# Performance work log

Hardware: AMD Instinct MI355X
Metric: run time of the kernel (lower is better)

The kernel has to match this reference:

```python
import jax, jax.numpy as jnp
import numpy as np

N = 10000      # nodes
E = 160000     # edges (avg degree 16)
D = 128        # channels
H = 4          # heads
C = 128        # per-head dim (PyG: out_channels per head = channels)
HC = H * C
EPS_SOFTMAX = 1e-16
EPS_NORM = 1e-5


def setup_inputs() -> dict:
    key = jax.random.key(0)
    ks = jax.random.split(key, 12)
    s = 1.0 / np.sqrt(D)
    sb = 1.0 / np.sqrt(3 * D)
    return {
        "x": jax.random.normal(ks[0], (N, D), jnp.float32),
        "edge_index": jax.random.randint(ks[1], (2, E), 0, N, dtype=jnp.int64),
        "Wq": jax.random.normal(ks[2], (D, HC), jnp.float32) * s,
        "bq": jnp.zeros((HC,), jnp.float32),
        "Wk": jax.random.normal(ks[3], (D, HC), jnp.float32) * s,
        "bk": jnp.zeros((HC,), jnp.float32),
        "Wv": jax.random.normal(ks[4], (D, HC), jnp.float32) * s,
        "bv": jnp.zeros((HC,), jnp.float32),
        "Wskip": jax.random.normal(ks[5], (D, D), jnp.float32) * s,
        "bskip": jnp.zeros((D,), jnp.float32),
        "Wbeta": jax.random.normal(ks[6], (3 * D,), jnp.float32) * sb,  # lin_beta, bias=False
        "gn_weight": jnp.ones((D,), jnp.float32),
        "gn_bias": jnp.zeros((D,), jnp.float32),
        "gn_mean_scale": jnp.ones((D,), jnp.float32),
    }


def reference(x, edge_index, Wq, bq, Wk, bk, Wv, bv, Wskip, bskip, Wbeta,
              gn_weight, gn_bias, gn_mean_scale):
    n = x.shape[0]
    src, dst = edge_index[0], edge_index[1]  # messages flow src(j) -> dst(i)

    # Projections [N,H,C]
    q = (x @ Wq + bq).reshape(n, H, C)
    k = (x @ Wk + bk).reshape(n, H, C)
    v = (x @ Wv + bv).reshape(n, H, C)

    # Per-edge attention logits [E,H]
    alpha = jnp.einsum('ehc,ehc->eh', q[dst], k[src]) / jnp.sqrt(jnp.float32(C))

    # Segment softmax over incoming edges of each dst node
    amax = jax.ops.segment_max(alpha, dst, num_segments=n)       # [N,H]
    amax = jnp.where(jnp.isfinite(amax), amax, 0.0)
    ex = jnp.exp(alpha - amax[dst])                              # [E,H]
    denom = jax.ops.segment_sum(ex, dst, num_segments=n)         # [N,H]
    attn = ex / (denom[dst] + EPS_SOFTMAX)                       # [E,H]

    # Weighted scatter-aggregate, then mean over heads (concat=False)
    msgs = attn[:, :, None] * v[src]                             # [E,H,C]
    out = jax.ops.segment_sum(msgs, dst, num_segments=n)         # [N,H,C]
    out = out.mean(axis=1)                                       # [N,D]

    # Beta-gated skip (PyG: beta = sigmoid(lin_beta([out, x_r, out - x_r])))
    skip = x @ Wskip + bskip
    beta = jax.nn.sigmoid(jnp.concatenate([out, skip, out - skip], axis=-1) @ Wbeta)
    beta = beta[:, None]
    out = beta * skip + (1.0 - beta) * out

    # GraphNorm (single graph): (x - mean_scale*mean) / sqrt(var + eps) * w + b
    mean = out.mean(axis=0)
    centered = out - gn_mean_scale * mean
    var = (centered * centered).mean(axis=0)
    out = gn_weight * centered / jnp.sqrt(var + EPS_NORM) + gn_bias

    # GELU (exact) + residual (shapes match); dropout is identity in eval
    out = jax.nn.gelu(out, approximate=False)
    return out + x
```

## Files before the change

### kernel.cpp

```cpp
#include <hip/hip_runtime.h>
#include <hip/hip_bf16.h>
#include <math.h>

#define D_DIM 128
#define HC_DIM 512

typedef __attribute__((ext_vector_type(8))) short bf16x8;
typedef __attribute__((ext_vector_type(4))) float f32x4;
typedef __attribute__((ext_vector_type(2))) float f32x2;

static __device__ __forceinline__ unsigned short f2bf(float f) {
  unsigned u = __float_as_uint(f);
  unsigned r = (u + 0x7fffu + ((u >> 16) & 1u)) >> 16;
  return (unsigned short)r;
}
static __device__ __forceinline__ float bflo(unsigned u) {
  return __uint_as_float(u << 16);
}
static __device__ __forceinline__ float bfhi(unsigned u) {
  return __uint_as_float(u & 0xffff0000u);
}

__global__ void prep_kernel(const float* __restrict__ x,
                            const float* __restrict__ Wq, const float* __restrict__ Wk,
                            const float* __restrict__ Wv, const float* __restrict__ Wskip,
                            const float* __restrict__ bq, const float* __restrict__ bk,
                            const float* __restrict__ bv, const float* __restrict__ bskip,
                            unsigned short* __restrict__ xb,
                            unsigned short* __restrict__ wcat,
                            float* __restrict__ bcat,
                            int* __restrict__ zbase, int zwords, int N) {
  int t = blockIdx.x * 256 + threadIdx.x;
  int X4 = N * 32;
  if (t < X4) {
    float4 f = *(const float4*)&x[t * 4];
    ushort4 o;
    o.x = f2bf(f.x); o.y = f2bf(f.y); o.z = f2bf(f.z); o.w = f2bf(f.w);
    *(ushort4*)&xb[t * 4] = o;
  } else if (t < X4 + 1664 * 128) {
    int widx = t - X4;
    if (widx < 3 * 65536) {
      int segi = widx >> 16;
      int r = widx & 65535;
      int kk = r >> 9;
      int m = r & 511;
      const float* W = (segi == 0) ? Wq : (segi == 1) ? Wk : Wv;
      wcat[(size_t)(segi * 512 + m) * 128 + kk] = f2bf(W[kk * 512 + m]);
    } else {
      int r = widx - 3 * 65536;
      int kk = r >> 7;
      int m = r & 127;
      wcat[(size_t)(1536 + m) * 128 + kk] = f2bf(Wskip[kk * 128 + m]);
    }
  } else if (t < X4 + 1664 * 128 + 1664) {
    int b = t - X4 - 1664 * 128;
    bcat[b] = (b < 512) ? bq[b] : (b < 1024) ? bk[b - 512]
            : (b < 1536) ? bv[b - 1024] : bskip[b - 1536];
  } else if (t < X4 + 1664 * 128 + 1664 + zwords) {
    zbase[t - X4 - 1664 * 128 - 1664] = 0;
  }
}

__global__ __launch_bounds__(256) void gemm_mfma_kernel(
    const unsigned short* __restrict__ Xb, const unsigned short* __restrict__ Wt,
    const float* __restrict__ bcat, unsigned short* __restrict__ qb,
    unsigned char* __restrict__ kv8, float* __restrict__ skip, int N) {
  const int tid = threadIdx.x;
  const int wave = tid >> 6, lane = tid & 63;
  const int l16 = lane & 15, quad = lane >> 4;
  const int row0 = (blockIdx.x * 4 + wave) * 64;
  const int col0 = blockIdx.y * 64;

  const unsigned short* xrow[4];
#pragma unroll
  for (int i = 0; i < 4; ++i) {
    int r = row0 + i * 16 + l16;
    if (r >= N) r = N - 1;
    xrow[i] = Xb + (size_t)r * 128;
  }
  const unsigned short* wrow[4];
  float bias[4];
#pragma unroll
  for (int j = 0; j < 4; ++j) {
    int c = col0 + j * 16 + l16;
    wrow[j] = Wt + (size_t)c * 128;
    bias[j] = bcat[c];
  }

  f32x4 acc[4][4] = {};
#pragma unroll
  for (int kk = 0; kk < 4; ++kk) {
    int k0 = kk * 32 + quad * 8;
    bf16x8 a[4], b[4];
#pragma unroll
    for (int i = 0; i < 4; ++i) a[i] = *(const bf16x8*)(xrow[i] + k0);
#pragma unroll
    for (int j = 0; j < 4; ++j) b[j] = *(const bf16x8*)(wrow[j] + k0);
#pragma unroll
    for (int i = 0; i < 4; ++i)
#pragma unroll
      for (int j = 0; j < 4; ++j)
        acc[i][j] = __builtin_amdgcn_mfma_f32_16x16x32_bf16(a[i], b[j], acc[i][j], 0, 0, 0);
  }

  const int kind = (col0 < 512) ? 0 : (col0 < 1536) ? 1 : 2;
#pragma unroll
  for (int i = 0; i < 4; ++i) {
#pragma unroll
    for (int reg = 0; reg < 4; ++reg) {
      int r = row0 + i * 16 + quad * 4 + reg;
      if (r < N) {
#pragma unroll
        for (int j = 0; j < 4; ++j) {
          int cidx = col0 + j * 16 + l16;
          float val = acc[i][j][reg] + bias[j];
          if (kind == 0) {
            qb[(size_t)r * 512 + cidx] = f2bf(val);
          } else if (kind == 1) {
            int pk = __builtin_amdgcn_cvt_pk_fp8_f32(val, val, 0, false);
            kv8[(size_t)r * 1024 + cidx - 512] = (unsigned char)pk;
          } else {
            skip[(size_t)r * 128 + cidx - 1536] = val;
          }
        }
      }
    }
  }
}

__global__ void hist_kernel(const int* __restrict__ dst, int* __restrict__ cnt, int E) {
  int e = blockIdx.x * 256 + threadIdx.x;
  if (e < E) atomicAdd(&cnt[dst[e]], 1);
}

__global__ __launch_bounds__(256) void scan1_kernel(const int* __restrict__ cnt,
                                                    int* __restrict__ off,
                                                    int* __restrict__ bsum, int n) {
  __shared__ int wsum[4];
  int tid = threadIdx.x;
  int i = blockIdx.x * 256 + tid;
  int lane = tid & 63, w = tid >> 6;
  int v = (i < n) ? cnt[i] : 0;
  int x = v;
#pragma unroll
  for (int d = 1; d < 64; d <<= 1) {
    int y = __shfl_up(x, d);
    if (lane >= d) x += y;
  }
  if (lane == 63) wsum[w] = x;
  __syncthreads();
  int wo = 0;
  for (int j = 0; j < w; ++j) wo += wsum[j];
  if (i < n) off[i] = wo + x - v;
  if (tid == 255) bsum[blockIdx.x] = wo + x;
}

__global__ __launch_bounds__(256) void scan23_kernel(int* __restrict__ off,
                                                     const int* __restrict__ bsum,
                                                     int nb, int n) {
  __shared__ int boffs[64];
  int tid = threadIdx.x;
  if (tid < 64) {
    int v = (tid < nb) ? bsum[tid] : 0;
    int x = v;
#pragma unroll
    for (int d = 1; d < 64; d <<= 1) {
      int y = __shfl_up(x, d);
      if (tid >= d) x += y;
    }
    boffs[tid] = x - v;
    if (tid == 63 && blockIdx.x == 0) off[n] = x;
  }
  __syncthreads();
  int i = blockIdx.x * 256 + tid;
  if (i < n) off[i] += boffs[blockIdx.x];
}

__global__ void scatter_kernel(const int* __restrict__ src, const int* __restrict__ dst,
                               const int* __restrict__ off, int* __restrict__ cur,
                               int* __restrict__ bsrc, int E) {
  int e = blockIdx.x * 256 + threadIdx.x;
  if (e < E) {
    int d = dst[e];
    int p = off[d] + atomicAdd(&cur[d], 1);
    bsrc[p] = src[e];
  }
}

__global__ __launch_bounds__(256) void attn_kernel(
    const unsigned short* __restrict__ qb, const unsigned char* __restrict__ kv8,
    const int* __restrict__ off, const int* __restrict__ bsrc,
    unsigned* __restrict__ oh, int N, int nper) {
  int bx = blockIdx.x;
  int head = bx / nper;
  int tid = threadIdx.x;
  int w = tid >> 6, lane = tid & 63;
  int node = (bx - head * nper) * 4 + w;
  if (node >= N) return;
  int g = lane >> 4, j = lane & 15;

  const float qscale = 0.08838834764831845f * 1.4426950408889634f;
  int4 qi = *(const int4*)(qb + (size_t)node * 512 + head * 128 + j * 8);
  float qf0 = bflo(qi.x) * qscale, qf1 = bfhi(qi.x) * qscale;
  float qf2 = bflo(qi.y) * qscale, qf3 = bfhi(qi.y) * qscale;
  float qf4 = bflo(qi.z) * qscale, qf5 = bfhi(qi.z) * qscale;
  float qf6 = bflo(qi.w) * qscale, qf7 = bfhi(qi.w) * qscale;

  const unsigned char* kb = kv8 + head * 128 + j * 8;
  int beg = off[node], end = off[node + 1];
  float lsum = 0.f;
  float o0 = 0.f, o1 = 0.f, o2 = 0.f, o3 = 0.f;
  float o4 = 0.f, o5 = 0.f, o6 = 0.f, o7 = 0.f;

  for (int idx = beg; idx < end; idx += 4) {
    int rem = end - idx;
    int e = bsrc[idx + ((g < rem) ? g : 0)];
    const unsigned char* kp = kb + (size_t)e * 1024;
    uint2 kw = *(const uint2*)kp;
    uint2 vw = *(const uint2*)(kp + 512);
    f32x2 k01 = __builtin_amdgcn_cvt_pk_f32_fp8(kw.x, false);
    f32x2 k23 = __builtin_amdgcn_cvt_pk_f32_fp8(kw.x, true);
    f32x2 k45 = __builtin_amdgcn_cvt_pk_f32_fp8(kw.y, false);
    f32x2 k67 = __builtin_amdgcn_cvt_pk_f32_fp8(kw.y, true);
    float p = qf0 * k01.x + qf1 * k01.y + qf2 * k23.x + qf3 * k23.y +
              qf4 * k45.x + qf5 * k45.y + qf6 * k67.x + qf7 * k67.y;
    p += __shfl_xor(p, 1);
    p += __shfl_xor(p, 2);
    p += __shfl_xor(p, 4);
    p += __shfl_xor(p, 8);
    float a = (g < rem) ? p : -1e30f;
    float wgt = exp2f(a);
    f32x2 v01 = __builtin_amdgcn_cvt_pk_f32_fp8(vw.x, false);
    f32x2 v23 = __builtin_amdgcn_cvt_pk_f32_fp8(vw.x, true);
    f32x2 v45 = __builtin_amdgcn_cvt_pk_f32_fp8(vw.y, false);
    f32x2 v67 = __builtin_amdgcn_cvt_pk_f32_fp8(vw.y, true);
    lsum += wgt;
    o0 += wgt * v01.x; o1 += wgt * v01.y;
    o2 += wgt * v23.x; o3 += wgt * v23.y;
    o4 += wgt * v45.x; o5 += wgt * v45.y;
    o6 += wgt * v67.x; o7 += wgt * v67.y;
  }
  o0 += __shfl_xor(o0, 16); o0 += __shfl_xor(o0, 32);
  o1 += __shfl_xor(o1, 16); o1 += __shfl_xor(o1, 32);
  o2 += __shfl_xor(o2, 16); o2 += __shfl_xor(o2, 32);
  o3 += __shfl_xor(o3, 16); o3 += __shfl_xor(o3, 32);
  o4 += __shfl_xor(o4, 16); o4 += __shfl_xor(o4, 32);
  o5 += __shfl_xor(o5, 16); o5 += __shfl_xor(o5, 32);
  o6 += __shfl_xor(o6, 16); o6 += __shfl_xor(o6, 32);
  o7 += __shfl_xor(o7, 16); o7 += __shfl_xor(o7, 32);
  lsum += __shfl_xor(lsum, 16); lsum += __shfl_xor(lsum, 32);
  float inv = 1.f / (lsum + 1e-16f);
  if (g == 0) {
    unsigned d0 = (unsigned)f2bf(o0 * inv) | ((unsigned)f2bf(o1 * inv) << 16);
    unsigned d1 = (unsigned)f2bf(o2 * inv) | ((unsigned)f2bf(o3 * inv) << 16);
    unsigned d2 = (unsigned)f2bf(o4 * inv) | ((unsigned)f2bf(o5 * inv) << 16);
    unsigned d3 = (unsigned)f2bf(o6 * inv) | ((unsigned)f2bf(o7 * inv) << 16);
    int4 st; st.x = (int)d0; st.y = (int)d1; st.z = (int)d2; st.w = (int)d3;
    *(int4*)(oh + ((size_t)head * N + node) * 64 + j * 4) = st;
  }
}

__global__ __launch_bounds__(256) void combine_kernel(
    const unsigned* __restrict__ oh, const float* __restrict__ skip,
    const float* __restrict__ Wbeta, float* __restrict__ out2,
    float* __restrict__ colsum, float* __restrict__ colsq, int N) {
  int tid = threadIdx.x;
  int lane = tid & 63, w = tid >> 6;
  int wid = blockIdx.x * 4 + w;
  float2 wb0 = *(const float2*)&Wbeta[lane * 2];
  float2 wb1 = *(const float2*)&Wbeta[128 + lane * 2];
  float2 wb2 = *(const float2*)&Wbeta[256 + lane * 2];
  float cs0 = 0.f, cq0 = 0.f, cs1 = 0.f, cq1 = 0.f;
#pragma unroll
  for (int k = 0; k < 4; ++k) {
    int n = wid + k * 2500;
    if (n < N) {
      unsigned h0 = oh[((size_t)0 * N + n) * 64 + lane];
      unsigned h1 = oh[((size_t)1 * N + n) * 64 + lane];
      unsigned h2 = oh[((size_t)2 * N + n) * 64 + lane];
      unsigned h3 = oh[((size_t)3 * N + n) * 64 + lane];
      float a0 = 0.25f * (bflo(h0) + bflo(h1) + bflo(h2) + bflo(h3));
      float a1 = 0.25f * (bfhi(h0) + bfhi(h1) + bfhi(h2) + bfhi(h3));
      float2 s = *(const float2*)&skip[(size_t)n * 128 + lane * 2];
      float p = a0 * wb0.x + s.x * wb1.x + (a0 - s.x) * wb2.x +
                a1 * wb0.y + s.y * wb1.y + (a1 - s.y) * wb2.y;
#pragma unroll
      for (int dmask = 1; dmask < 64; dmask <<= 1) p += __shfl_xor(p, dmask);
      float beta = 1.f / (1.f + __expf(-p));
      float o0 = beta * s.x + (1.f - beta) * a0;
      float o1 = beta * s.y + (1.f - beta) * a1;
      float2 ov; ov.x = o0; ov.y = o1;
      *(float2*)&out2[(size_t)n * 128 + lane * 2] = ov;
      cs0 += o0; cq0 += o0 * o0;
      cs1 += o1; cq1 += o1 * o1;
    }
  }
  __shared__ float red[4][128];
  __shared__ float redq[4][128];
  red[w][lane * 2] = cs0;
  red[w][lane * 2 + 1] = cs1;
  redq[w][lane * 2] = cq0;
  redq[w][lane * 2 + 1] = cq1;
  __syncthreads();
  if (w == 0) {
    int c = lane * 2;
    float s0 = red[0][c] + red[1][c] + red[2][c] + red[3][c];
    float s1 = red[0][c + 1] + red[1][c + 1] + red[2][c + 1] + red[3][c + 1];
    float q0 = redq[0][c] + redq[1][c] + redq[2][c] + redq[3][c];
    float q1 = redq[0][c + 1] + redq[1][c + 1] + redq[2][c + 1] + redq[3][c + 1];
    atomicAdd(&colsum[c], s0);
    atomicAdd(&colsum[c + 1], s1);
    atomicAdd(&colsq[c], q0);
    atomicAdd(&colsq[c + 1], q1);
  }
}

__global__ void final_kernel(const float* __restrict__ out2,
                             const float* __restrict__ colsum,
                             const float* __restrict__ colsq,
                             const float* __restrict__ gnw,
                             const float* __restrict__ gnb,
                             const float* __restrict__ gnms,
                             const float* __restrict__ x,
                             float* __restrict__ y, int total2, float invN) {
  int i = blockIdx.x * 256 + threadIdx.x;
  if (i < total2) {
    int c = (i & 63) * 2;
    float2 cs = *(const float2*)&colsum[c];
    float2 cq = *(const float2*)&colsq[c];
    float2 gw = *(const float2*)&gnw[c];
    float2 gb = *(const float2*)&gnb[c];
    float2 gs = *(const float2*)&gnms[c];
    float mean0 = cs.x * invN, mean1 = cs.y * invN;
    float var0 = cq.x * invN - mean0 * mean0 * gs.x * (2.f - gs.x);
    float var1 = cq.y * invN - mean1 * mean1 * gs.y * (2.f - gs.y);
    float mul0 = gw.x / sqrtf(var0 + 1e-5f);
    float mul1 = gw.y / sqrtf(var1 + 1e-5f);
    float2 o = *(const float2*)&out2[i * 2];
    float2 xx = *(const float2*)&x[i * 2];
    float t0 = (o.x - gs.x * mean0) * mul0 + gb.x;
    float t1 = (o.y - gs.y * mean1) * mul1 + gb.y;
    float g0 = 0.5f * t0 * (1.f + erff(t0 * 0.70710678118654752f));
    float g1 = 0.5f * t1 * (1.f + erff(t1 * 0.70710678118654752f));
    float2 r; r.x = g0 + xx.x; r.y = g1 + xx.y;
    *(float2*)&y[i * 2] = r;
  }
}

extern "C" void kernel_launch(void* const* d_in, const int* in_sizes, int n_in,
                              void* d_out, int out_size, void* d_ws, size_t ws_size,
                              hipStream_t stream) {
  const float* x     = (const float*)d_in[0];
  const int*   ei    = (const int*)d_in[1];
  const float* Wq    = (const float*)d_in[2];
  const float* bq    = (const float*)d_in[3];
  const float* Wk    = (const float*)d_in[4];
  const float* bk    = (const float*)d_in[5];
  const float* Wv    = (const float*)d_in[6];
  const float* bv    = (const float*)d_in[7];
  const float* Wskip = (const float*)d_in[8];
  const float* bskip = (const float*)d_in[9];
  const float* Wbeta = (const float*)d_in[10];
  const float* gnw   = (const float*)d_in[11];
  const float* gnb   = (const float*)d_in[12];
  const float* gnms  = (const float*)d_in[13];

  const int N = in_sizes[0] / D_DIM;
  const int E = in_sizes[1] / 2;
  const int* src = ei;
  const int* dst = ei + E;

  char* p = (char*)d_ws;
  unsigned short* qb  = (unsigned short*)p; p += (size_t)N * 512 * 2;
  unsigned char*  kv8 = (unsigned char*)p;  p += (size_t)N * 1024;
  unsigned*       oh  = (unsigned*)p;       p += (size_t)4 * N * 64 * 4;
  float*          skip = (float*)p;         p += (size_t)N * 128 * 4;
  float*          out2 = (float*)p;         p += (size_t)N * 128 * 4;
  int*   cnt    = (int*)p;   p += (size_t)N * 4;
  int*   cur    = (int*)p;   p += (size_t)N * 4;
  float* colsum = (float*)p; p += 128 * 4;
  float* colsq  = (float*)p; p += 128 * 4;
  int zwords = 2 * N + 256;
  int* off    = (int*)p;   p += (size_t)(N + 16) * 4;
  int* bsum   = (int*)p;   p += 64 * 4;
  int* bsrc   = (int*)p;   p += (size_t)E * 4;
  unsigned short* wcat = (unsigned short*)p; p += (size_t)1664 * 128 * 2;
  float* bcat = (float*)p; p += 1664 * 4;
  unsigned short* xb = (unsigned short*)oh;

  int prepTotal = N * 32 + 1664 * 128 + 1664 + zwords;
  prep_kernel<<<(prepTotal + 255) / 256, 256, 0, stream>>>(
      x, Wq, Wk, Wv, Wskip, bq, bk, bv, bskip, xb, wcat, bcat, cnt, zwords, N);

  gemm_mfma_kernel<<<dim3(40, 26), 256, 0, stream>>>(
      xb, wcat, bcat, qb, kv8, skip, N);

  int eBlocks = (E + 255) / 256;
  hist_kernel<<<eBlocks, 256, 0, stream>>>(dst, cnt, E);

  int nBlocks = (N + 255) / 256;
  scan1_kernel<<<nBlocks, 256, 0, stream>>>(cnt, off, bsum, N);
  scan23_kernel<<<nBlocks, 256, 0, stream>>>(off, bsum, nBlocks, N);

  scatter_kernel<<<eBlocks, 256, 0, stream>>>(src, dst, off, cur, bsrc, E);

  int nper = (N + 3) / 4;
  attn_kernel<<<nper * 4, 256, 0, stream>>>(qb, kv8, off, bsrc, oh, N, nper);

  combine_kernel<<<625, 256, 0, stream>>>(oh, skip, Wbeta, out2, colsum, colsq, N);

  int total2 = N * D_DIM / 2;
  final_kernel<<<(total2 + 255) / 256, 256, 0, stream>>>(
      out2, colsum, colsq, gnw, gnb, gnms, x, (float*)d_out, total2, 1.f / (float)N);
}
```

Measured before the change: 216.1 us.

## Fuse degree histogram into GEMM, single-block scan, fp16 keys with dot2

Moves the per-edge degree histogram atomics into the projection GEMM kernel, and replaces the two-kernel scan with a single 1024-thread block. Together these remove two launches. Keys are now stored as fp16 in their own array, separate from fp8 values, and the q·k dot product uses packed fdot2 instead of fp8 unpacking and scalar FMAs. The cost is twice the key gather bytes per edge and a serial single-block scan. The change also buys better key precision.

```diff
diff --git a/kernel.cpp b/kernel.cpp
--- a/kernel.cpp
+++ b/kernel.cpp
@@ -8,6 +8,7 @@
 typedef __attribute__((ext_vector_type(8))) short bf16x8;
 typedef __attribute__((ext_vector_type(4))) float f32x4;
 typedef __attribute__((ext_vector_type(2))) float f32x2;
+typedef __attribute__((ext_vector_type(2))) _Float16 h16x2;
 
 static __device__ __forceinline__ unsigned short f2bf(float f) {
   unsigned u = __float_as_uint(f);
@@ -64,8 +65,18 @@
 __global__ __launch_bounds__(256) void gemm_mfma_kernel(
     const unsigned short* __restrict__ Xb, const unsigned short* __restrict__ Wt,
     const float* __restrict__ bcat, unsigned short* __restrict__ qb,
-    unsigned char* __restrict__ kv8, float* __restrict__ skip, int N) {
+    unsigned short* __restrict__ kf, unsigned char* __restrict__ v8,
+    float* __restrict__ skip,
+    const int* __restrict__ dst, int* __restrict__ cnt, int N, int E) {
   const int tid = threadIdx.x;
+  {
+    int nblk = gridDim.x * gridDim.y;
+    int lb = blockIdx.y * gridDim.x + blockIdx.x;
+    int per = (E + nblk - 1) / nblk;
+    int e0 = lb * per;
+    int e1 = min(e0 + per, E);
+    for (int e = e0 + tid; e < e1; e += 256) atomicAdd(&cnt[dst[e]], 1);
+  }
   const int wave = tid >> 6, lane = tid & 63;
   const int l16 = lane & 15, quad = lane >> 4;
   const int row0 = (blockIdx.x * 4 + wave) * 64;
@@ -103,7 +114,7 @@
         acc[i][j] = __builtin_amdgcn_mfma_f32_16x16x32_bf16(a[i], b[j], acc[i][j], 0, 0, 0);
   }
 
-  const int kind = (col0 < 512) ? 0 : (col0 < 1536) ? 1 : 2;
+  const int kind = (col0 < 512) ? 0 : (col0 < 1024) ? 1 : (col0 < 1536) ? 2 : 3;
 #pragma unroll
   for (int i = 0; i < 4; ++i) {
 #pragma unroll
@@ -117,8 +128,11 @@
           if (kind == 0) {
             qb[(size_t)r * 512 + cidx] = f2bf(val);
           } else if (kind == 1) {
+            _Float16 hv = (_Float16)val;
+            kf[(size_t)r * 512 + cidx - 512] = *(unsigned short*)&hv;
+          } else if (kind == 2) {
             int pk = __builtin_amdgcn_cvt_pk_fp8_f32(val, val, 0, false);
-            kv8[(size_t)r * 1024 + cidx - 512] = (unsigned char)pk;
+            v8[(size_t)r * 512 + cidx - 1024] = (unsigned char)pk;
           } else {
             skip[(size_t)r * 128 + cidx - 1536] = val;
           }
@@ -128,52 +142,34 @@
   }
 }
 
-__global__ void hist_kernel(const int* __restrict__ dst, int* __restrict__ cnt, int E) {
-  int e = blockIdx.x * 256 + threadIdx.x;
-  if (e < E) atomicAdd(&cnt[dst[e]], 1);
-}
-
-__global__ __launch_bounds__(256) void scan1_kernel(const int* __restrict__ cnt,
-                                                    int* __restrict__ off,
-                                                    int* __restrict__ bsum, int n) {
-  __shared__ int wsum[4];
+__global__ __launch_bounds__(1024) void scan_kernel(const int* __restrict__ cnt,
+                                                    int* __restrict__ off, int n) {
+  __shared__ int wsum[16];
+  __shared__ int carry;
   int tid = threadIdx.x;
-  int i = blockIdx.x * 256 + tid;
   int lane = tid & 63, w = tid >> 6;
-  int v = (i < n) ? cnt[i] : 0;
-  int x = v;
-#pragma unroll
-  for (int d = 1; d < 64; d <<= 1) {
-    int y = __shfl_up(x, d);
-    if (lane >= d) x += y;
-  }
-  if (lane == 63) wsum[w] = x;
+  if (tid == 0) carry = 0;
   __syncthreads();
-  int wo = 0;
-  for (int j = 0; j < w; ++j) wo += wsum[j];
-  if (i < n) off[i] = wo + x - v;
-  if (tid == 255) bsum[blockIdx.x] = wo + x;
-}
-
-__global__ __launch_bounds__(256) void scan23_kernel(int* __restrict__ off,
-                                                     const int* __restrict__ bsum,
-                                                     int nb, int n) {
-  __shared__ int boffs[64];
-  int tid = threadIdx.x;
-  if (tid < 64) {
-    int v = (tid < nb) ? bsum[tid] : 0;
+  for (int base = 0; base < n; base += 1024) {
+    int i = base + tid;
+    int v = (i < n) ? cnt[i] : 0;
     int x = v;
 #pragma unroll
     for (int d = 1; d < 64; d <<= 1) {
       int y = __shfl_up(x, d);
-      if (tid >= d) x += y;
+      if (lane >= d) x += y;
     }
-    boffs[tid] = x - v;
-    if (tid == 63 && blockIdx.x == 0) off[n] = x;
-  }
-  __syncthreads();
-  int i = blockIdx.x * 256 + tid;
-  if (i < n) off[i] += boffs[blockIdx.x];
+    if (lane == 63) wsum[w] = x;
+    __syncthreads();
+    int wo = 0;
+    for (int jj = 0; jj < w; ++jj) wo += wsum[jj];
+    int c = carry;
+    if (i < n) off[i] = c + wo + x - v;
+    __syncthreads();
+    if (tid == 1023) carry = c + wo + x;
+    __syncthreads();
+  }
+  if (tid == 0) off[n] = carry;
 }
 
 __global__ void scatter_kernel(const int* __restrict__ src, const int* __restrict__ dst,
@@ -188,9 +184,9 @@
 }
 
 __global__ __launch_bounds__(256) void attn_kernel(
-    const unsigned short* __restrict__ qb, const unsigned char* __restrict__ kv8,
-    const int* __restrict__ off, const int* __restrict__ bsrc,
-    unsigned* __restrict__ oh, int N, int nper) {
+    const unsigned short* __restrict__ qb, const unsigned short* __restrict__ kf,
+    const unsigned char* __restrict__ v8, const int* __restrict__ off,
+    const int* __restrict__ bsrc, unsigned* __restrict__ oh, int N, int nper) {
   int bx = blockIdx.x;
   int head = bx / nper;
   int tid = threadIdx.x;
@@ -201,12 +197,14 @@
 
   const float qscale = 0.08838834764831845f * 1.4426950408889634f;
   int4 qi = *(const int4*)(qb + (size_t)node * 512 + head * 128 + j * 8);
-  float qf0 = bflo(qi.x) * qscale, qf1 = bfhi(qi.x) * qscale;
-  float qf2 = bflo(qi.y) * qscale, qf3 = bfhi(qi.y) * qscale;
-  float qf4 = bflo(qi.z) * qscale, qf5 = bfhi(qi.z) * qscale;
-  float qf6 = bflo(qi.w) * qscale, qf7 = bfhi(qi.w) * qscale;
-
-  const unsigned char* kb = kv8 + head * 128 + j * 8;
+  h16x2 qh0, qh1, qh2, qh3;
+  qh0[0] = (_Float16)(bflo(qi.x) * qscale); qh0[1] = (_Float16)(bfhi(qi.x) * qscale);
+  qh1[0] = (_Float16)(bflo(qi.y) * qscale); qh1[1] = (_Float16)(bfhi(qi.y) * qscale);
+  qh2[0] = (_Float16)(bflo(qi.z) * qscale); qh2[1] = (_Float16)(bfhi(qi.z) * qscale);
+  qh3[0] = (_Float16)(bflo(qi.w) * qscale); qh3[1] = (_Float16)(bfhi(qi.w) * qscale);
+
+  const unsigned short* kb = kf + head * 128 + j * 8;
+  const unsigned char* vb = v8 + head * 128 + j * 8;
   int beg = off[node], end = off[node + 1];
   float lsum = 0.f;
   float o0 = 0.f, o1 = 0.f, o2 = 0.f, o3 = 0.f;
@@ -215,15 +213,12 @@
   for (int idx = beg; idx < end; idx += 4) {
     int rem = end - idx;
     int e = bsrc[idx + ((g < rem) ? g : 0)];
-    const unsigned char* kp = kb + (size_t)e * 1024;
-    uint2 kw = *(const uint2*)kp;
-    uint2 vw = *(const uint2*)(kp + 512);
-    f32x2 k01 = __builtin_amdgcn_cvt_pk_f32_fp8(kw.x, false);
-    f32x2 k23 = __builtin_amdgcn_cvt_pk_f32_fp8(kw.x, true);
-    f32x2 k45 = __builtin_amdgcn_cvt_pk_f32_fp8(kw.y, false);
-    f32x2 k67 = __builtin_amdgcn_cvt_pk_f32_fp8(kw.y, true);
-    float p = qf0 * k01.x + qf1 * k01.y + qf2 * k23.x + qf3 * k23.y +
-              qf4 * k45.x + qf5 * k45.y + qf6 * k67.x + qf7 * k67.y;
+    uint4 kw = *(const uint4*)(kb + (size_t)e * 512);
+    uint2 vw = *(const uint2*)(vb + (size_t)e * 512);
+    float p = __builtin_amdgcn_fdot2(qh0, *(h16x2*)&kw.x, 0.f, false);
+    p = __builtin_amdgcn_fdot2(qh1, *(h16x2*)&kw.y, p, false);
+    p = __builtin_amdgcn_fdot2(qh2, *(h16x2*)&kw.z, p, false);
+    p = __builtin_amdgcn_fdot2(qh3, *(h16x2*)&kw.w, p, false);
     p += __shfl_xor(p, 1);
     p += __shfl_xor(p, 2);
     p += __shfl_xor(p, 4);
@@ -371,18 +366,18 @@
   const int* dst = ei + E;
 
   char* p = (char*)d_ws;
-  unsigned short* qb  = (unsigned short*)p; p += (size_t)N * 512 * 2;
-  unsigned char*  kv8 = (unsigned char*)p;  p += (size_t)N * 1024;
-  unsigned*       oh  = (unsigned*)p;       p += (size_t)4 * N * 64 * 4;
-  float*          skip = (float*)p;         p += (size_t)N * 128 * 4;
-  float*          out2 = (float*)p;         p += (size_t)N * 128 * 4;
+  unsigned short* qb = (unsigned short*)p; p += (size_t)N * 512 * 2;
+  unsigned short* kf = (unsigned short*)p; p += (size_t)N * 512 * 2;
+  unsigned char*  v8 = (unsigned char*)p;  p += (size_t)N * 512;
+  unsigned*       oh = (unsigned*)p;       p += (size_t)4 * N * 64 * 4;
+  float*          skip = (float*)p;        p += (size_t)N * 128 * 4;
+  float*          out2 = (float*)p;        p += (size_t)N * 128 * 4;
   int*   cnt    = (int*)p;   p += (size_t)N * 4;
   int*   cur    = (int*)p;   p += (size_t)N * 4;
   float* colsum = (float*)p; p += 128 * 4;
   float* colsq  = (float*)p; p += 128 * 4;
   int zwords = 2 * N + 256;
   int* off    = (int*)p;   p += (size_t)(N + 16) * 4;
-  int* bsum   = (int*)p;   p += 64 * 4;
   int* bsrc   = (int*)p;   p += (size_t)E * 4;
   unsigned short* wcat = (unsigned short*)p; p += (size_t)1664 * 128 * 2;
   float* bcat = (float*)p; p += 1664 * 4;
@@ -393,19 +388,15 @@
       x, Wq, Wk, Wv, Wskip, bq, bk, bv, bskip, xb, wcat, bcat, cnt, zwords, N);
 
   gemm_mfma_kernel<<<dim3(40, 26), 256, 0, stream>>>(
-      xb, wcat, bcat, qb, kv8, skip, N);
+      xb, wcat, bcat, qb, kf, v8, skip, dst, cnt, N, E);
+
+  scan_kernel<<<1, 1024, 0, stream>>>(cnt, off, N);
 
   int eBlocks = (E + 255) / 256;
-  hist_kernel<<<eBlocks, 256, 0, stream>>>(dst, cnt, E);
-
-  int nBlocks = (N + 255) / 256;
-  scan1_kernel<<<nBlocks, 256, 0, stream>>>(cnt, off, bsum, N);
-  scan23_kernel<<<nBlocks, 256, 0, stream>>>(off, bsum, nBlocks, N);
-
   scatter_kernel<<<eBlocks, 256, 0, stream>>>(src, dst, off, cur, bsrc, E);
 
   int nper = (N + 3) / 4;
-  attn_kernel<<<nper * 4, 256, 0, stream>>>(qb, kv8, off, bsrc, oh, N, nper);
+  attn_kernel<<<nper * 4, 256, 0, stream>>>(qb, kf, v8, off, bsrc, oh, N, nper);
 
   combine_kernel<<<625, 256, 0, stream>>>(oh, skip, Wbeta, out2, colsum, colsq, N);
 
```

Result: no change. 219.7 us (+1.7%).
